# Performance work log

Measured on AMD Instinct MI355X. Metric: run time of the kernel, lower is better.

The kernel has to match this reference:

```python
import jax, jax.numpy as jnp
import numpy as np

B, S, D, E, H = 4, 2048, 1024, 8, 2048


def setup_inputs() -> dict:
    key = jax.random.key(0)
    ks = jax.random.split(key, 8)
    s_in = 1.0 / np.sqrt(D)   # torch Linear default init scale (uniform bound)
    s_hid = 1.0 / np.sqrt(H)
    return {
        "x": jax.random.normal(ks[0], (B, S, D), dtype=jnp.float32),
        "W1": jax.random.uniform(ks[1], (E, D, H), minval=-s_in, maxval=s_in, dtype=jnp.float32),
        "b1": jax.random.uniform(ks[2], (E, H), minval=-s_in, maxval=s_in, dtype=jnp.float32),
        "W2": jax.random.uniform(ks[3], (E, H, D), minval=-s_hid, maxval=s_hid, dtype=jnp.float32),
        "b2": jax.random.uniform(ks[4], (E, D), minval=-s_hid, maxval=s_hid, dtype=jnp.float32),
        "Wg": jax.random.uniform(ks[5], (D, E), minval=-s_in, maxval=s_in, dtype=jnp.float32),
        "bg": jax.random.uniform(ks[6], (E,), minval=-s_in, maxval=s_in, dtype=jnp.float32),
    }


def reference(x, W1, b1, W2, b2, Wg, bg):
    # All-experts dense MoE (eval mode: dropout is identity).
    # hidden: [B,S,E,H]
    h = jax.nn.relu(jnp.einsum("bsd,edh->bseh", x, W1) + b1)
    # expert outputs: [B,S,E,D]
    expert_out = jnp.einsum("bseh,ehd->bsed", h, W2) + b2
    # gate (raw linear, no softmax in original): [B,S,E]
    gate = jnp.einsum("bsd,de->bse", x, Wg) + bg
    # gate-weighted sum over experts -> [B,S,D]
    return jnp.einsum("bse,bsed->bsd", gate, expert_out)
```

## Files before the change

kernel.cpp:

```cpp
#include <hip/hip_runtime.h>

#define NTOK 8192
#define DDIM 1024
#define HDIM 2048
#define NEXP 8

#define BM 256
#define BN 128
#define BK 64

typedef unsigned short u16;
typedef short bf16x8 __attribute__((ext_vector_type(8)));
typedef float f32x4 __attribute__((ext_vector_type(4)));
typedef float float4_t __attribute__((ext_vector_type(4)));

__device__ __forceinline__ u16 f2bf(float f) {
  unsigned u = __float_as_uint(f);
  u += 0x7FFFu + ((u >> 16) & 1u);
  return (u16)(u >> 16);
}

#define GLOAD_LDS16(gp, lp)                                                     \
  __builtin_amdgcn_global_load_lds(                                             \
      (const __attribute__((address_space(1))) unsigned int*)(gp),              \
      (__attribute__((address_space(3))) unsigned int*)(lp), 16, 0, 0)

__global__ void k_prep(const float* __restrict__ x, const float* __restrict__ Wg,
                       const float* __restrict__ bg,
                       u16* __restrict__ xb, float* __restrict__ gate) {
  const int tok = (blockIdx.x * 256 + threadIdx.x) >> 6;
  const int lane = threadIdx.x & 63;
  const float* xr = x + (size_t)tok * DDIM;
  u16* xo = xb + (size_t)tok * DDIM;
  float s[NEXP];
#pragma unroll
  for (int e = 0; e < NEXP; ++e) s[e] = 0.f;
#pragma unroll
  for (int it = 0; it < 2; ++it) {
    const int d0 = lane * 8 + it * 512;
    float4_t v0 = *(const float4_t*)(xr + d0);
    float4_t v1 = *(const float4_t*)(xr + d0 + 4);
    union { bf16x8 v; u16 h[8]; } u;
    u.h[0] = f2bf(v0.x); u.h[1] = f2bf(v0.y); u.h[2] = f2bf(v0.z); u.h[3] = f2bf(v0.w);
    u.h[4] = f2bf(v1.x); u.h[5] = f2bf(v1.y); u.h[6] = f2bf(v1.z); u.h[7] = f2bf(v1.w);
    *(bf16x8*)(xo + d0) = u.v;
    float xv[8] = {v0.x, v0.y, v0.z, v0.w, v1.x, v1.y, v1.z, v1.w};
#pragma unroll
    for (int j = 0; j < 8; ++j) {
      const float4_t w0 = *(const float4_t*)(Wg + (size_t)(d0 + j) * NEXP);
      const float4_t w1 = *(const float4_t*)(Wg + (size_t)(d0 + j) * NEXP + 4);
      s[0] += xv[j] * w0.x; s[1] += xv[j] * w0.y;
      s[2] += xv[j] * w0.z; s[3] += xv[j] * w0.w;
      s[4] += xv[j] * w1.x; s[5] += xv[j] * w1.y;
      s[6] += xv[j] * w1.z; s[7] += xv[j] * w1.w;
    }
  }
#pragma unroll
  for (int off = 32; off; off >>= 1)
#pragma unroll
    for (int e = 0; e < NEXP; ++e) s[e] += __shfl_down(s[e], off);
  if (lane == 0) {
#pragma unroll
    for (int e = 0; e < NEXP; ++e) gate[(size_t)tok * NEXP + e] = s[e] + bg[e];
  }
}

__global__ void k_transpose(const float* __restrict__ in, u16* __restrict__ out,
                            int R, int C, size_t oexp, int orstride) {
  __shared__ float t[64][65];
  const int rb = blockIdx.x * 64, cb = blockIdx.y * 64;
  const float* pin = in + (size_t)blockIdx.z * R * C;
  u16* pout = out + (size_t)blockIdx.z * oexp;
  const int tid = threadIdx.x;
  {
    const int r = tid >> 4;
    const int c4 = (tid & 15) * 4;
#pragma unroll
    for (int i = 0; i < 4; ++i) {
      float4_t v = *(const float4_t*)(pin + (size_t)(rb + r + 16 * i) * C + cb + c4);
      t[r + 16 * i][c4 + 0] = v.x;
      t[r + 16 * i][c4 + 1] = v.y;
      t[r + 16 * i][c4 + 2] = v.z;
      t[r + 16 * i][c4 + 3] = v.w;
    }
  }
  __syncthreads();
  {
    const int oc = tid >> 3;
    const int r8 = (tid & 7) * 8;
#pragma unroll
    for (int jp = 0; jp < 2; ++jp) {
      const int ocol = oc + 32 * jp;
      union { bf16x8 v; u16 h[8]; } u;
#pragma unroll
      for (int k = 0; k < 8; ++k) u.h[k] = f2bf(t[r8 + k][ocol]);
      *(bf16x8*)(pout + (size_t)(cb + ocol) * orstride + rb + r8) = u.v;
    }
  }
}

template <int MODE>
__global__ __launch_bounds__(512, 2) void k_gemm(
    const u16* __restrict__ A, int lda,
    const u16* __restrict__ Bt, int ldb,
    const float* __restrict__ bias,
    const float* __restrict__ gate, int ebase,
    void* __restrict__ Cout, int ldc,
    int tilesN, int K, int accum) {
  __shared__ __align__(16) u16 lds[3 * (BM + BN) * BK];
  const int tid = threadIdx.x;
  const int lane = tid & 63;
  const int wid = tid >> 6;
  const int wm = wid >> 1;
  const int wn = wid & 1;

  int nwg = gridDim.x, wg = blockIdx.x;
  int q = nwg >> 3, r8 = nwg & 7;
  int xcd = wg & 7, lo = wg >> 3;
  int swz = (xcd < r8 ? xcd * (q + 1) : r8 * (q + 1) + (xcd - r8) * q) + lo;
  int tm = swz / tilesN, tn = swz % tilesN;
  int bm = tm * BM, bn = tn * BN;

  const int srow = tid >> 3;
  const int scol = ((tid & 7) ^ (srow & 7)) << 3;
  const u16* gA = A + (size_t)(bm + srow) * lda + scol;
  const u16* gB = Bt + (size_t)(bn + srow) * ldb + scol;
  const int dofs = wid * 512;

  u16* a0 = lds;            u16* b0 = lds + BM * BK;
  u16* a1 = b0 + BN * BK;   u16* b1p = a1 + BM * BK;
  u16* a2 = b1p + BN * BK;  u16* b2p = a2 + BM * BK;

#define STAGE(aD, bD, kt)                                                       \
  {                                                                             \
    const u16* sa_ = gA + (size_t)(kt) * BK;                                    \
    const u16* sb_ = gB + (size_t)(kt) * BK;                                    \
    GLOAD_LDS16(sa_,                       (aD) + dofs);                        \
    GLOAD_LDS16(sa_ + (size_t)64 * lda,    (aD) + 4096 + dofs);                 \
    GLOAD_LDS16(sa_ + (size_t)128 * lda,   (aD) + 8192 + dofs);                 \
    GLOAD_LDS16(sa_ + (size_t)192 * lda,   (aD) + 12288 + dofs);                \
    GLOAD_LDS16(sb_,                       (bD) + dofs);                        \
    GLOAD_LDS16(sb_ + (size_t)64 * ldb,    (bD) + 4096 + dofs);                 \
  }

  const int fr = lane & 15;
  const int fq = lane >> 4;
  const int xr = fr & 7;
  const int so0 = ((0 + fq) ^ xr) << 3;
  const int so1 = ((4 + fq) ^ xr) << 3;
  int aro[4], bro[4];
#pragma unroll
  for (int m = 0; m < 4; ++m) aro[m] = (wm * 64 + m * 16 + fr) << 6;
#pragma unroll
  for (int n = 0; n < 4; ++n) bro[n] = (wn * 64 + n * 16 + fr) << 6;

  f32x4 acc[4][4] = {};
  const int nkt = K >> 6;

  STAGE(a0, b0, 0);
  STAGE(a1, b1p, 1);
  asm volatile("s_waitcnt vmcnt(6)" ::: "memory");
  __builtin_amdgcn_s_barrier();
  __builtin_amdgcn_sched_barrier(0);

  u16 *aC = a0, *bC = b0, *aN = a1, *bN = b1p, *aF = a2, *bF = b2p;

#pragma unroll 1
  for (int t = 0; t < nkt; ++t) {
    if (t + 2 < nkt) STAGE(aF, bF, t + 2);
#pragma unroll
    for (int kk = 0; kk < 2; ++kk) {
      const int so = kk ? so1 : so0;
      bf16x8 af[4], bfv[4];
#pragma unroll
      for (int m = 0; m < 4; ++m) af[m] = *(const bf16x8*)(aC + aro[m] + so);
#pragma unroll
      for (int n = 0; n < 4; ++n) bfv[n] = *(const bf16x8*)(bC + bro[n] + so);
      __builtin_amdgcn_s_setprio(1);
#pragma unroll
      for (int m = 0; m < 4; ++m)
#pragma unroll
        for (int n = 0; n < 4; ++n)
          acc[m][n] = __builtin_amdgcn_mfma_f32_16x16x32_bf16(af[m], bfv[n],
                                                              acc[m][n], 0, 0, 0);
      __builtin_amdgcn_s_setprio(0);
    }
    if (t != nkt - 1) {
      if (t + 2 < nkt) {
        asm volatile("s_waitcnt vmcnt(6)" ::: "memory");
      } else {
        asm volatile("s_waitcnt vmcnt(0)" ::: "memory");
      }
      __builtin_amdgcn_s_barrier();
      __builtin_amdgcn_sched_barrier(0);
      u16* tp;
      tp = aC; aC = aN; aN = aF; aF = tp;
      tp = bC; bC = bN; bN = bF; bF = tp;
    }
  }

  const int colbase = bn + wn * 64 + fr;
  if (MODE == 1) {
    const int e = ebase + ((bn + wn * 64) >> 11);
    float bcol[4];
#pragma unroll
    for (int n = 0; n < 4; ++n) bcol[n] = bias[colbase + n * 16];
    u16* O = (u16*)Cout;
#pragma unroll
    for (int m = 0; m < 4; ++m) {
#pragma unroll
      for (int j = 0; j < 4; ++j) {
        int r = bm + wm * 64 + m * 16 + fq * 4 + j;
        float g = gate[(size_t)r * NEXP + e];
#pragma unroll
        for (int n = 0; n < 4; ++n) {
          float v = fmaxf(acc[m][n][j] + bcol[n], 0.f) * g;
          O[(size_t)r * ldc + colbase + n * 16] = f2bf(v);
        }
      }
    }
  } else {
    float* O = (float*)Cout;
    float b2c[4][NEXP];
    if (!accum) {
#pragma unroll
      for (int n = 0; n < 4; ++n)
#pragma unroll
        for (int e = 0; e < NEXP; ++e)
          b2c[n][e] = bias[(size_t)e * DDIM + colbase + n * 16];
    }
#pragma unroll
    for (int m = 0; m < 4; ++m) {
#pragma unroll
      for (int j = 0; j < 4; ++j) {
        int r = bm + wm * 64 + m * 16 + fq * 4 + j;
        if (!accum) {
          float g8[NEXP];
#pragma unroll
          for (int e = 0; e < NEXP; ++e) g8[e] = gate[(size_t)r * NEXP + e];
#pragma unroll
          for (int n = 0; n < 4; ++n) {
            float v = acc[m][n][j];
#pragma unroll
            for (int e = 0; e < NEXP; ++e) v += g8[e] * b2c[n][e];
            O[(size_t)r * DDIM + colbase + n * 16] = v;
          }
        } else {
#pragma unroll
          for (int n = 0; n < 4; ++n) {
            size_t idx = (size_t)r * DDIM + colbase + n * 16;
            O[idx] += acc[m][n][j];
          }
        }
      }
    }
  }
#undef STAGE
}

extern "C" void kernel_launch(void* const* d_in, const int* in_sizes, int n_in,
                              void* d_out, int out_size, void* d_ws, size_t ws_size,
                              hipStream_t stream) {
  (void)in_sizes; (void)n_in; (void)out_size;
  const float* x  = (const float*)d_in[0];
  const float* W1 = (const float*)d_in[1];
  const float* b1 = (const float*)d_in[2];
  const float* W2 = (const float*)d_in[3];
  const float* b2 = (const float*)d_in[4];
  const float* Wg = (const float*)d_in[5];
  const float* bg = (const float*)d_in[6];
  float* out = (float*)d_out;

  size_t o_xb   = 0;
  size_t o_w1t  = o_xb  + (size_t)NTOK * DDIM * 2;
  size_t o_w2t  = o_w1t + (size_t)NEXP * HDIM * DDIM * 2;
  size_t o_gate = o_w2t + (size_t)NEXP * DDIM * HDIM * 2;
  size_t o_h    = o_gate + (size_t)NTOK * NEXP * 4;
  size_t base   = o_h;

  int G = 8;
  while (G > 1 && base + (size_t)NTOK * G * HDIM * 2 > ws_size) G >>= 1;
  if (base + (size_t)NTOK * G * HDIM * 2 > ws_size) return;

  u16*   xb   = (u16*)((char*)d_ws + o_xb);
  u16*   W1t  = (u16*)((char*)d_ws + o_w1t);
  u16*   W2t  = (u16*)((char*)d_ws + o_w2t);
  float* gate = (float*)((char*)d_ws + o_gate);
  u16*   hbuf = (u16*)((char*)d_ws + o_h);

  k_prep<<<NTOK / 4, 256, 0, stream>>>(x, Wg, bg, xb, gate);
  dim3 g1(DDIM / 64, HDIM / 64, NEXP);
  k_transpose<<<g1, 256, 0, stream>>>(W1, W1t, DDIM, HDIM, (size_t)HDIM * DDIM, DDIM);
  dim3 g2(HDIM / 64, DDIM / 64, NEXP);
  k_transpose<<<g2, 256, 0, stream>>>(W2, W2t, HDIM, DDIM, (size_t)HDIM, NEXP * HDIM);

  const int rounds = NEXP / G;
  for (int g = 0; g < rounds; ++g) {
    const int Ng = G * HDIM;
    k_gemm<1><<<(NTOK / BM) * (Ng / BN), 512, 0, stream>>>(
        xb, DDIM, W1t + (size_t)g * Ng * DDIM, DDIM,
        b1 + (size_t)g * Ng, gate, g * G,
        hbuf, Ng, Ng / BN, DDIM, 0);
    k_gemm<2><<<(NTOK / BM) * (DDIM / BN), 512, 0, stream>>>(
        hbuf, Ng, W2t + (size_t)g * Ng, NEXP * HDIM,
        b2, gate, 0,
        out, DDIM, DDIM / BN, Ng, g > 0);
  }
}
```

Baseline: 687.7 us.

## Process experts in fixed groups of two with per-expert W2t layout

Fixes the expert group size at two instead of using as many experts as the workspace allows, so the hidden buffer is smaller and more likely to stay cached between the two GEMMs. W2 is now transposed into a per-expert [D][H] layout, and the second GEMM's B-operand address jumps to the next expert's block every 32 K-tiles. This costs more launches and more read-modify-write passes over the output accumulator, but shrinks the hidden-activation working set.

```diff
diff --git a/kernel.cpp b/kernel.cpp
--- a/kernel.cpp
+++ b/kernel.cpp
@@ -4,6 +4,7 @@
 #define DDIM 1024
 #define HDIM 2048
 #define NEXP 8
+#define GEXP 2
 
 #define BM 256
 #define BN 128
@@ -99,7 +100,7 @@
   }
 }
 
-template <int MODE>
+template <int MODE, int BCH>
 __global__ __launch_bounds__(512, 2) void k_gemm(
     const u16* __restrict__ A, int lda,
     const u16* __restrict__ Bt, int ldb,
@@ -131,10 +132,14 @@
   u16* a1 = b0 + BN * BK;   u16* b1p = a1 + BM * BK;
   u16* a2 = b1p + BN * BK;  u16* b2p = a2 + BM * BK;
 
+#define BOFF(kt) (BCH ? ((size_t)((kt) >> 5) * ((size_t)DDIM * HDIM) +          \
+                         (size_t)((kt) & 31) * BK)                              \
+                      : (size_t)(kt) * BK)
+
 #define STAGE(aD, bD, kt)                                                       \
   {                                                                             \
     const u16* sa_ = gA + (size_t)(kt) * BK;                                    \
-    const u16* sb_ = gB + (size_t)(kt) * BK;                                    \
+    const u16* sb_ = gB + BOFF(kt);                                             \
     GLOAD_LDS16(sa_,                       (aD) + dofs);                        \
     GLOAD_LDS16(sa_ + (size_t)64 * lda,    (aD) + 4096 + dofs);                 \
     GLOAD_LDS16(sa_ + (size_t)128 * lda,   (aD) + 8192 + dofs);                 \
@@ -256,6 +261,7 @@
     }
   }
 #undef STAGE
+#undef BOFF
 }
 
 extern "C" void kernel_launch(void* const* d_in, const int* in_sizes, int n_in,
@@ -276,11 +282,8 @@
   size_t o_w2t  = o_w1t + (size_t)NEXP * HDIM * DDIM * 2;
   size_t o_gate = o_w2t + (size_t)NEXP * DDIM * HDIM * 2;
   size_t o_h    = o_gate + (size_t)NTOK * NEXP * 4;
-  size_t base   = o_h;
-
-  int G = 8;
-  while (G > 1 && base + (size_t)NTOK * G * HDIM * 2 > ws_size) G >>= 1;
-  if (base + (size_t)NTOK * G * HDIM * 2 > ws_size) return;
+  size_t need   = o_h   + (size_t)NTOK * GEXP * HDIM * 2;
+  if (ws_size < need) return;
 
   u16*   xb   = (u16*)((char*)d_ws + o_xb);
   u16*   W1t  = (u16*)((char*)d_ws + o_w1t);
@@ -292,17 +295,16 @@
   dim3 g1(DDIM / 64, HDIM / 64, NEXP);
   k_transpose<<<g1, 256, 0, stream>>>(W1, W1t, DDIM, HDIM, (size_t)HDIM * DDIM, DDIM);
   dim3 g2(HDIM / 64, DDIM / 64, NEXP);
-  k_transpose<<<g2, 256, 0, stream>>>(W2, W2t, HDIM, DDIM, (size_t)HDIM, NEXP * HDIM);
-
-  const int rounds = NEXP / G;
-  for (int g = 0; g < rounds; ++g) {
-    const int Ng = G * HDIM;
-    k_gemm<1><<<(NTOK / BM) * (Ng / BN), 512, 0, stream>>>(
+  k_transpose<<<g2, 256, 0, stream>>>(W2, W2t, HDIM, DDIM, (size_t)DDIM * HDIM, HDIM);
+
+  const int Ng = GEXP * HDIM;
+  for (int g = 0; g < NEXP / GEXP; ++g) {
+    k_gemm<1, 0><<<(NTOK / BM) * (Ng / BN), 512, 0, stream>>>(
         xb, DDIM, W1t + (size_t)g * Ng * DDIM, DDIM,
-        b1 + (size_t)g * Ng, gate, g * G,
+        b1 + (size_t)g * Ng, gate, g * GEXP,
         hbuf, Ng, Ng / BN, DDIM, 0);
-    k_gemm<2><<<(NTOK / BM) * (DDIM / BN), 512, 0, stream>>>(
-        hbuf, Ng, W2t + (size_t)g * Ng, NEXP * HDIM,
+    k_gemm<2, 1><<<(NTOK / BM) * (DDIM / BN), 512, 0, stream>>>(
+        hbuf, Ng, W2t + (size_t)g * GEXP * DDIM * HDIM, HDIM,
         b2, gate, 0,
         out, DDIM, DDIM / BN, Ng, g > 0);
   }
```

After: 705.5 us. +2.6%, slower.
